# Performance work log

Hardware: AMD Instinct MI355X
Metric: run time of the kernel (lower is better)

The kernel has to match this reference:

```python
import jax, jax.numpy as jnp
import numpy as np

C = 1024        # number of classes
N = 8           # proxies per class
ALLNUM = C * N  # 8192 total proxies
DIM = 512
R = 0.05
TOPK = int(np.ceil(R * ALLNUM))  # 410
LAM = 0.3
B = 2048


def setup_inputs() -> dict:
    key = jax.random.key(0)
    k1, k2, k3 = jax.random.split(key, 3)
    inp = jax.random.normal(k1, (B, DIM), dtype=jnp.float32)
    target = jax.random.randint(k2, (B,), 0, C, dtype=jnp.int64)
    # kaiming-uniform-initialized proxies approximated by scaled normal init
    proxies = jax.random.normal(k3, (DIM, ALLNUM), dtype=jnp.float32)
    instance_label = jnp.repeat(jnp.arange(C, dtype=jnp.int64), N)  # [ALLNUM]
    return {"input": inp, "target": target, "Proxies": proxies,
            "instance_label": instance_label}


def reference(input, target, Proxies, instance_label):
    # L2-normalize each proxy column (F.normalize along dim=0, eps=1e-12)
    norm = jnp.maximum(jnp.linalg.norm(Proxies, axis=0, keepdims=True), 1e-12)
    centers = Proxies / norm                             # [DIM, ALLNUM]
    similarity = input @ centers                          # [B, ALLNUM]

    positive_mask = (target[:, None] == instance_label[None, :]).astype(similarity.dtype)
    _, indices = jax.lax.top_k(similarity + 1000.0 * positive_mask, TOPK)  # [B, TOPK]

    rows = jnp.arange(similarity.shape[0])[:, None]
    mask = jnp.zeros_like(similarity).at[rows, indices].set(1.0)
    prob_a = mask * similarity                            # sparse-masked similarities

    y_instance_onehot = jax.nn.one_hot(instance_label, C, dtype=similarity.dtype)  # [ALLNUM, C]
    logits = prob_a @ y_instance_onehot                   # [B, C]

    y_target_onehot = jax.nn.one_hot(target, C, dtype=similarity.dtype)  # [B, C]
    logits_mask = 1.0 - (logits == 0.0).astype(similarity.dtype)

    # scale_mask_softmax with scale=1 along dim=1
    e = jnp.exp(logits) * logits_mask
    predict = e / (1e-8 + jnp.sum(e, axis=1, keepdims=True))
    lossClassify = jnp.mean(jnp.sum(-y_target_onehot * jnp.log(predict + 1e-20), axis=1))

    # proxy regularizer: cross-entropy of proxy-vs-class logits
    simCenter = centers.T @ centers                       # [ALLNUM, ALLNUM]
    centers_logits = simCenter @ y_instance_onehot        # [ALLNUM, C]
    logp = jax.nn.log_softmax(centers_logits, axis=1)
    reg = -jnp.mean(jnp.take_along_axis(logp, instance_label[:, None], axis=1))

    return (lossClassify + LAM * reg, lossClassify)
```

## Files before the change

### kernel.cpp

```cpp
#include <hip/hip_runtime.h>
#include <hip/hip_bf16.h>
#include <math.h>

#define C_CLS   1024
#define NPROXY  8
#define ALLNUM  8192
#define DIM     512
#define TOPK    410
#define LAM     0.3f
#define BATCH   2048

#define BAND_CAP_BLK 28
#define ROW_CAP      512
#define GCAP         64

typedef __bf16 bf16x8 __attribute__((ext_vector_type(8)));
typedef float floatx4 __attribute__((ext_vector_type(4)));
typedef unsigned short ushort_t;

#define WS_RNORM 0
#define WS_SIG   8192
#define WS_LP    10240
#define WS_RP    12288
#define WS_CNT   14336
#define WS_NDEF  16384
#define WS_FLAG  18432
#define WS_CLS   20480
#define WS_BVAL  (WS_CLS + 2048*1024)
#define WS_BCOL  (WS_BVAL + 2048*512)
#define WS_ABF   (WS_BCOL + 2048*256)
#define WS_PBF   (WS_ABF + 524288)
#define WS_STBF  (WS_PBF + 2097152)
#define WS_MX    (WS_STBF + 262144)
#define WS_SE    (WS_MX + 65536)
#define WS_DIAG  (WS_SE + 65536)

__device__ inline float block_reduce(float v, int is_max, float* red, int t) {
    #pragma unroll
    for (int o = 32; o > 0; o >>= 1) {
        float w = __shfl_down(v, o);
        v = is_max ? fmaxf(v, w) : (v + w);
    }
    __syncthreads();
    if ((t & 63) == 0) red[t >> 6] = v;
    __syncthreads();
    return is_max ? fmaxf(fmaxf(red[0], red[1]), fmaxf(red[2], red[3]))
                  : (red[0] + red[1] + red[2] + red[3]);
}

__device__ inline ushort_t f2bf(float f) {
    unsigned u = __float_as_uint(f);
    return (ushort_t)((u + 0x7FFFu + ((u >> 16) & 1u)) >> 16);
}

__device__ inline float bf2f(ushort_t u) {
    return __uint_as_float(((unsigned)u) << 16);
}

__device__ inline void ld_g2l_16(const void* g, void* l) {
    __builtin_amdgcn_global_load_lds(
        (const __attribute__((address_space(1))) unsigned int*)g,
        (__attribute__((address_space(3))) unsigned int*)l,
        16, 0, 0);
}

__device__ inline unsigned f2ord(float f) {
    unsigned u = __float_as_uint(f);
    return (u & 0x80000000u) ? ~u : (u | 0x80000000u);
}

__global__ __launch_bounds__(256) void k_prep1(const float* __restrict__ P,
                                               const float* __restrict__ input,
                                               float* __restrict__ rnorm,
                                               float* __restrict__ rowsig,
                                               ushort_t* __restrict__ Abf,
                                               ushort_t* __restrict__ Pbf,
                                               ushort_t* __restrict__ Stbf,
                                               unsigned* __restrict__ zaux) {
    __shared__ float stile[512 * 33];
    __shared__ float cred[256];
    __shared__ float s_rn[32];
    int bx = blockIdx.x, t = threadIdx.x;
    if (bx < 256) {
        int c0 = bx * 32;
        #pragma unroll
        for (int it = 0; it < 16; ++it) {
            int r = it * 32 + (t >> 3);
            int c4 = (t & 7) * 4;
            float4 v = *(const float4*)&P[(size_t)r * ALLNUM + c0 + c4];
            stile[r * 33 + c4]     = v.x;
            stile[r * 33 + c4 + 1] = v.y;
            stile[r * 33 + c4 + 2] = v.z;
            stile[r * 33 + c4 + 3] = v.w;
        }
        __syncthreads();
        int tc = t & 31, g = t >> 5;
        float s = 0.f;
        #pragma unroll 8
        for (int k = 0; k < 64; ++k) {
            float v = stile[(g * 64 + k) * 33 + tc];
            s += v * v;
        }
        cred[g * 32 + tc] = s;
        __syncthreads();
        if (g == 0) {
            float tot = 0.f;
            #pragma unroll
            for (int k = 0; k < 8; ++k) tot += cred[k * 32 + tc];
            float r = 1.0f / fmaxf(sqrtf(tot), 1e-12f);
            rnorm[c0 + tc] = r;
            s_rn[tc] = r;
        }
        __syncthreads();
        #pragma unroll
        for (int p = 0; p < 16; ++p) {
            int idx = t + 256 * p;
            int c = idx >> 7, d4 = (idx & 127) * 4;
            ushort4 o;
            o.x = f2bf(stile[(d4    ) * 33 + c]);
            o.y = f2bf(stile[(d4 + 1) * 33 + c]);
            o.z = f2bf(stile[(d4 + 2) * 33 + c]);
            o.w = f2bf(stile[(d4 + 3) * 33 + c]);
            *(ushort4*)&Pbf[(size_t)(c0 + c) * DIM + d4] = o;
        }
        #pragma unroll
        for (int p = 0; p < 4; ++p) {
            int idx = t + 256 * p;
            int cc = idx >> 8, d2 = (idx & 255) * 2;
            float v0 = 0.f, v1 = 0.f;
            #pragma unroll
            for (int n = 0; n < 8; ++n) {
                float rr = s_rn[cc * 8 + n];
                v0 += stile[(d2    ) * 33 + cc * 8 + n] * rr;
                v1 += stile[(d2 + 1) * 33 + cc * 8 + n] * rr;
            }
            ushort2 o; o.x = f2bf(v0); o.y = f2bf(v1);
            *(ushort2*)&Stbf[(size_t)(bx * 4 + cc) * DIM + d2] = o;
        }
    } else if (bx < 256 + 1024) {
        int a = bx - 256;
        int idx = a * 256 + t;
        float4 v = ((const float4*)input)[idx];
        ushort4 o;
        o.x = f2bf(v.x); o.y = f2bf(v.y); o.z = f2bf(v.z); o.w = f2bf(v.w);
        ((ushort4*)Abf)[idx] = o;
        float sq = v.x * v.x + v.y * v.y + v.z * v.z + v.w * v.w;
        #pragma unroll
        for (int off = 32; off > 0; off >>= 1) sq += __shfl_down(sq, off);
        int lane = t & 63, w = t >> 6;
        if (lane == 0) cred[w] = sq;
        __syncthreads();
        if (t == 0) {
            rowsig[2 * a]     = sqrtf(cred[0] + cred[1]);
            rowsig[2 * a + 1] = sqrtf(cred[2] + cred[3]);
        }
    } else {
        for (int i = t; i < 3 * 2048; i += 256) zaux[i] = 0u;
    }
}

__global__ __launch_bounds__(512, 1) void k_gemms(const ushort_t* __restrict__ Abf,
                                                  const ushort_t* __restrict__ Pbf,
                                                  const ushort_t* __restrict__ Stbf,
                                                  const float* __restrict__ rnorm,
                                                  const float* __restrict__ rowsig,
                                                  const int* __restrict__ target,
                                                  float* __restrict__ g_cls,
                                                  float* __restrict__ g_bval,
                                                  ushort_t* __restrict__ g_bcol,
                                                  unsigned* __restrict__ g_cnt,
                                                  unsigned* __restrict__ g_ndef,
                                                  unsigned* __restrict__ g_flag,
                                                  float* __restrict__ g_mx,
                                                  float* __restrict__ g_se,
                                                  float* __restrict__ g_diag) {
    __shared__ __align__(16) ushort_t smem[73728];
    int bx = blockIdx.x, t = threadIdx.x;
    int w = t >> 6, lane = t & 63;
    int ml = lane & 15, q4 = lane >> 4;
    int wm = w >> 1, wn = w & 1;

    int wid = (bx & 7) * 96 + (bx >> 3);
    int isg0 = (wid < 512);
    const ushort_t* Ap;
    const ushort_t* Bp;
    int bi, bj;
    if (isg0) {
        bi = (wid & 7) * 256;
        bj = (wid >> 3) * 128;
        Ap = Abf; Bp = Pbf;
    } else {
        int id1 = wid - 512;
        bi = (id1 & 31) * 256;
        bj = (id1 >> 5) * 128;
        Ap = Pbf; Bp = Stbf;
    }

    floatx4 acc[4][4];
    #pragma unroll
    for (int mf = 0; mf < 4; ++mf)
        #pragma unroll
        for (int nf = 0; nf < 4; ++nf)
            acc[mf][nf] = (floatx4){0.f, 0.f, 0.f, 0.f};

    #define STAGE(t_, k0_) do {                                                \
        int bo_ = ((t_) % 3) * 24576;                                          \
        _Pragma("unroll")                                                      \
        for (int it_ = 0; it_ < 4; ++it_) {                                    \
            int c_ = w * 256 + it_ * 64 + lane;                                \
            int m_ = c_ >> 3, q_ = (c_ & 7) ^ (m_ & 7);                        \
            ld_g2l_16(Ap + ((size_t)(bi + m_) << 9) + (k0_) + q_ * 8,          \
                      &smem[bo_ + c_ * 8]);                                    \
        }                                                                      \
        _Pragma("unroll")                                                      \
        for (int it_ = 0; it_ < 2; ++it_) {                                    \
            int c_ = w * 128 + it_ * 64 + lane;                                \
            int m_ = c_ >> 3, q_ = (c_ & 7) ^ (m_ & 7);                        \
            ld_g2l_16(Bp + ((size_t)(bj + m_) << 9) + (k0_) + q_ * 8,          \
                      &smem[bo_ + 16384 + c_ * 8]);                            \
        } } while (0)

    STAGE(0, 0);
    STAGE(1, 64);

    #pragma unroll
    for (int tt = 0; tt < 8; ++tt) {
        if (tt < 7) asm volatile("s_waitcnt vmcnt(6)" ::: "memory");
        else        asm volatile("s_waitcnt vmcnt(0)" ::: "memory");
        __builtin_amdgcn_s_barrier();
        if (tt < 6) STAGE(tt + 2, (tt + 2) * 64);

        const ushort_t* Xa = &smem[(tt % 3) * 24576];
        const ushort_t* Xb = Xa + 16384;
        bf16x8 af[2][4], bfr[2][4];
        #pragma unroll
        for (int kk = 0; kk < 2; ++kk) {
            #pragma unroll
            for (int nf = 0; nf < 4; ++nf) {
                int n = wn * 64 + nf * 16 + ml;
                int s = (kk * 4 + q4) ^ (n & 7);
                bfr[kk][nf] = *(const bf16x8*)&Xb[n * 64 + s * 8];
            }
            #pragma unroll
            for (int mf = 0; mf < 4; ++mf) {
                int m = wm * 64 + mf * 16 + ml;
                int s = (kk * 4 + q4) ^ (m & 7);
                af[kk][mf] = *(const bf16x8*)&Xa[m * 64 + s * 8];
            }
        }
        __builtin_amdgcn_s_setprio(1);
        #pragma unroll
        for (int kk = 0; kk < 2; ++kk)
            #pragma unroll
            for (int mf = 0; mf < 4; ++mf)
                #pragma unroll
                for (int nf = 0; nf < 4; ++nf)
                    acc[mf][nf] = __builtin_amdgcn_mfma_f32_16x16x32_bf16(
                        af[kk][mf], bfr[kk][nf], acc[mf][nf], 0, 0, 0);
        __builtin_amdgcn_s_setprio(0);
    }
    #undef STAGE
    __syncthreads();

    if (isg0) {
        unsigned char* sb8 = (unsigned char*)smem;
        float*    e_cls = (float*)sb8;
        float*    e_bv  = (float*)(sb8 + 16384);
        ushort_t* e_bc  = (ushort_t*)(sb8 + 45056);
        unsigned* e_cnt = (unsigned*)(sb8 + 59392);
        unsigned* e_nd  = (unsigned*)(sb8 + 60416);

        #pragma unroll
        for (int i = t; i < 4096; i += 512) e_cls[i] = 0.f;
        if (t < 256) { e_cnt[t] = 0u; e_nd[t] = 0u; }
        __syncthreads();

        #pragma unroll
        for (int mf = 0; mf < 4; ++mf) {
            int rl0 = wm * 64 + mf * 16 + q4 * 4;
            int rowb = bi + rl0;
            float4 rs4 = *(const float4*)&rowsig[rowb];
            int4   tg4 = *(const int4*)&target[rowb];
            #pragma unroll
            for (int nf = 0; nf < 4; ++nf) {
                int cl = wn * 64 + nf * 16 + ml;
                int col = bj + cl;
                float sc = rnorm[col];
                int cls = col >> 3;
                int clsl = cl >> 3;
                #pragma unroll
                for (int i = 0; i < 4; ++i) {
                    int rl = rl0 + i;
                    float v = acc[mf][nf][i] * sc;
                    float sg = ((const float*)&rs4)[i] * (1.0f / 22.616f);
                    float hiT = 1.80f * sg, loT = 1.47f * sg;
                    int tg = ((const int*)&tg4)[i];
                    if (cls == tg) {
                        atomicAdd(&e_cls[rl * 16 + clsl], v);
                    } else if (v >= hiT) {
                        atomicAdd(&e_cls[rl * 16 + clsl], v);
                        atomicAdd(&e_nd[rl], 1u);
                    } else if (v >= loT) {
                        unsigned u = atomicAdd(&e_cnt[rl], 1u);
                        if (u < BAND_CAP_BLK) {
                            e_bv[rl * BAND_CAP_BLK + u] = v;
                            e_bc[rl * BAND_CAP_BLK + u] = (ushort_t)col;
                        }
                    }
                }
            }
        }
        __syncthreads();

        int bjc = bj >> 3;
        #pragma unroll
        for (int i = t; i < 4096; i += 512) {
            int rl = i >> 4, c = i & 15;
            g_cls[(size_t)(bi + rl) * C_CLS + bjc + c] = e_cls[i];
        }
        if (t < 256) {
            int row = bi + t;
            unsigned cbb = e_cnt[t];
            unsigned nd = e_nd[t];
            if (nd) atomicAdd(&g_ndef[row], nd);
            if (cbb) {
                unsigned cc = (cbb > BAND_CAP_BLK) ? BAND_CAP_BLK : cbb;
                unsigned base = atomicAdd(&g_cnt[row], cc);
                if (cbb > BAND_CAP_BLK || base + cc > ROW_CAP) g_flag[row] = 1u;
                for (unsigned j = 0; j < cc; ++j) {
                    if (base + j >= ROW_CAP) break;
                    g_bval[(size_t)row * ROW_CAP + base + j] = e_bv[t * BAND_CAP_BLK + j];
                    g_bcol[(size_t)row * ROW_CAP + base + j] = e_bc[t * BAND_CAP_BLK + j];
                }
            }
        }
    } else {
        int cj = bj >> 7;
        float mloc[4][4], sloc[4][4];
        #pragma unroll
        for (int mf = 0; mf < 4; ++mf) {
            int rowb = bi + wm * 64 + mf * 16 + q4 * 4;
            float4 rnr = *(const float4*)&rnorm[rowb];
            #pragma unroll
            for (int i = 0; i < 4; ++i) {
                float mm = -1e30f;
                #pragma unroll
                for (int nf = 0; nf < 4; ++nf)
                    mm = fmaxf(mm, acc[mf][nf][i] * ((const float*)&rnr)[i]);
                mloc[mf][i] = mm;
            }
        }
        #pragma unroll
        for (int off = 1; off < 16; off <<= 1)
            #pragma unroll
            for (int mf = 0; mf < 4; ++mf)
                #pragma unroll
                for (int i = 0; i < 4; ++i)
                    mloc[mf][i] = fmaxf(mloc[mf][i], __shfl_xor(mloc[mf][i], off));
        #pragma unroll
        for (int mf = 0; mf < 4; ++mf) {
            int rowb = bi + wm * 64 + mf * 16 + q4 * 4;
            float4 rnr = *(const float4*)&rnorm[rowb];
            #pragma unroll
            for (int i = 0; i < 4; ++i) {
                float ss = 0.f;
                int row = rowb + i;
                #pragma unroll
                for (int nf = 0; nf < 4; ++nf) {
                    float v = acc[mf][nf][i] * ((const float*)&rnr)[i];
                    ss += expf(v - mloc[mf][i]);
                    int col = bj + wn * 64 + nf * 16 + ml;
                    if (col == (row >> 3)) g_diag[row] = v;
                }
                sloc[mf][i] = ss;
            }
        }
        #pragma unroll
        for (int off = 1; off < 16; off <<= 1)
            #pragma unroll
            for (int mf = 0; mf < 4; ++mf)
                #pragma unroll
                for (int i = 0; i < 4; ++i)
                    sloc[mf][i] += __shfl_xor(sloc[mf][i], off);
        float* s_m = (float*)smem;
        float* s_s = s_m + 512;
        if (ml == 0) {
            #pragma unroll
            for (int mf = 0; mf < 4; ++mf)
                #pragma unroll
                for (int i = 0; i < 4; ++i) {
                    int r = wm * 64 + mf * 16 + q4 * 4 + i;
                    s_m[r * 2 + wn] = mloc[mf][i];
                    s_s[r * 2 + wn] = sloc[mf][i];
                }
        }
        __syncthreads();
        if (t < 256) {
            float m0 = s_m[2 * t], m1 = s_m[2 * t + 1];
            float s0 = s_s[2 * t], s1 = s_s[2 * t + 1];
            float M = fmaxf(m0, m1);
            float S = s0 * expf(m0 - M) + s1 * expf(m1 - M);
            g_mx[(size_t)(bi + t) * 8 + cj] = M;
            g_se[(size_t)(bi + t) * 8 + cj] = S;
        }
    }
}

__device__ inline void suffix_select1(unsigned* s_hist, unsigned kk,
                                      unsigned* s_wtot, unsigned* sh_bin,
                                      unsigned* sh_k, int t, int lane, int wid) {
    unsigned h = s_hist[t];
    unsigned v = h;
    #pragma unroll
    for (int off = 1; off < 64; off <<= 1) {
        unsigned o = __shfl_down(v, off);
        if (lane + off < 64) v += o;
    }
    if (lane == 0) s_wtot[wid] = v;
    __syncthreads();
    unsigned above = v - h;
    for (int w2 = wid + 1; w2 < 4; ++w2) above += s_wtot[w2];
    unsigned cum = above + h;
    if (cum >= kk && above < kk) { *sh_bin = (unsigned)t; *sh_k = kk - above; }
    __syncthreads();
}

__global__ __launch_bounds__(256) void k_finish(const int* __restrict__ target,
                                                const float* __restrict__ rowsig,
                                                const float* __restrict__ rnorm,
                                                const ushort_t* __restrict__ Abf,
                                                const ushort_t* __restrict__ Pbf,
                                                const float* __restrict__ g_cls,
                                                const float* __restrict__ g_bval,
                                                const ushort_t* __restrict__ g_bcol,
                                                const unsigned* __restrict__ g_cnt,
                                                const unsigned* __restrict__ g_ndef,
                                                const unsigned* __restrict__ g_flag,
                                                float* __restrict__ loss_part,
                                                const float* __restrict__ g_mx,
                                                const float* __restrict__ g_se,
                                                const float* __restrict__ g_diag,
                                                float* __restrict__ reg_part) {
    __shared__ __align__(16) unsigned char smem[16384];
    int bx = blockIdx.x, t = threadIdx.x;
    int lane = t & 63, wid = t >> 6;

    if (bx < 2048) {
        float*    s_cls  = (float*)smem;
        float*    s_bval = (float*)(smem + 4096);
        ushort_t* s_bcol = (ushort_t*)(smem + 6144);
        unsigned* s_hist = (unsigned*)(smem + 7168);
        float*    s_arow = (float*)(smem + 8192);
        unsigned* s_wtot = (unsigned*)(smem + 10240);
        unsigned* shv    = (unsigned*)(smem + 10256);
        float*    shf    = (float*)(smem + 10272);
        float*    red    = (float*)(smem + 10288);
        float*    s_gval = (float*)(smem + 10304);

        int b = bx;
        int tgt = target[b];
        float sig = rowsig[b] * (1.0f / 22.616f);
        float hiT = 1.80f * sig, loT = 1.47f * sig;
        float binscale = 256.0f / (hiT - loT);

        ((float4*)s_cls)[t] = ((const float4*)(g_cls + (size_t)b * C_CLS))[t];
        unsigned cnt = g_cnt[b], nd = g_ndef[b], fl = g_flag[b];
        int kq = (TOPK - NPROXY) - (int)nd;
        int ok = (fl == 0u) && (cnt <= ROW_CAP) && (kq >= 0) && ((int)cnt >= kq);
        if (t == 0) shv[1] = 0u;
        s_hist[t] = 0u;
        __syncthreads();

        if (ok) {
            if (kq > 0) {
                for (int j = t; j < (int)cnt; j += 256) {
                    float v = g_bval[(size_t)b * ROW_CAP + j];
                    s_bval[j] = v;
                    s_bcol[j] = g_bcol[(size_t)b * ROW_CAP + j];
                    int bin = (int)((v - loT) * binscale);
                    bin = (bin > 255) ? 255 : bin;
                    atomicAdd(&s_hist[bin], 1u);
                }
                __syncthreads();
                suffix_select1(s_hist, (unsigned)kq, s_wtot, &shv[2], &shv[3], t, lane, wid);
                int Bb = (int)shv[2];
                int knew = (int)shv[3];
                for (int j = t; j < (int)cnt; j += 256) {
                    float v = s_bval[j];
                    int bin = (int)((v - loT) * binscale);
                    bin = (bin > 255) ? 255 : bin;
                    if (bin == Bb) {
                        unsigned g = atomicAdd(&shv[1], 1u);
                        if (g < GCAP) s_gval[g] = v;
                    }
                }
                __syncthreads();
                int gc = (int)shv[1];
                if (gc <= GCAP) {
                    if (t < gc) {
                        float vj = s_gval[t];
                        unsigned g = 0, geq = 0;
                        for (int i = 0; i < gc; ++i) {
                            float vi = s_gval[i];
                            g   += (vi > vj) ? 1u : 0u;
                            geq += (vi >= vj) ? 1u : 0u;
                        }
                        if (g < (unsigned)knew && geq >= (unsigned)knew) shf[0] = vj;
                    }
                } else {
                    for (int j = t; j < (int)cnt; j += 256) {
                        float vj = s_bval[j];
                        unsigned g = 0, geq = 0;
                        for (int i = 0; i < (int)cnt; ++i) {
                            float vi = s_bval[i];
                            g   += (vi > vj) ? 1u : 0u;
                            geq += (vi >= vj) ? 1u : 0u;
                        }
                        if (g < (unsigned)kq && geq >= (unsigned)kq) shf[0] = vj;
                    }
                }
                __syncthreads();
                float thr = shf[0];
                for (int j = t; j < (int)cnt; j += 256)
                    if (s_bval[j] >= thr)
                        atomicAdd(&s_cls[s_bcol[j] >> 3], s_bval[j]);
            }
        } else {
            for (int i = t; i < DIM; i += 256)
                s_arow[i] = bf2f(Abf[(size_t)b * DIM + i]);
            #pragma unroll
            for (int i = 0; i < 4; ++i) s_cls[t + 256 * i] = 0.f;
            __syncthreads();
            float4 v4[8];
            for (int p = 0; p < 8; ++p) {
                int f = t + 256 * p;
                float vv[4];
                for (int e = 0; e < 4; ++e) {
                    int col = 4 * f + e;
                    const ushort_t* pc = Pbf + (size_t)col * DIM;
                    float a = 0.f;
                    for (int d = 0; d < DIM; ++d)
                        a += s_arow[d] * bf2f(pc[d]);
                    vv[e] = a * rnorm[col];
                }
                float4 o; o.x = vv[0]; o.y = vv[1]; o.z = vv[2]; o.w = vv[3];
                v4[p] = o;
            }
            #pragma unroll
            for (int p = 0; p < 8; ++p) {
                int f = t + 256 * p;
                const float* pv = (const float*)&v4[p];
                if ((f >> 1) == tgt)
                    atomicAdd(&s_cls[tgt], pv[0] + pv[1] + pv[2] + pv[3]);
            }
            unsigned L = 0u, R = 0xFFFFFFFFu;
            for (int it = 0; it < 33 && R - L > 1; ++it) {
                unsigned mid = L + ((R - L) >> 1);
                float c = 0.f;
                #pragma unroll
                for (int p = 0; p < 8; ++p) {
                    int f = t + 256 * p;
                    const float* pv = (const float*)&v4[p];
                    if ((f >> 1) != tgt) {
                        #pragma unroll
                        for (int e = 0; e < 4; ++e)
                            c += (f2ord(pv[e]) >= mid) ? 1.f : 0.f;
                    }
                }
                c = block_reduce(c, 0, red, t);
                if (c >= (float)(TOPK - NPROXY)) L = mid; else R = mid;
                __syncthreads();
            }
            #pragma unroll
            for (int p = 0; p < 8; ++p) {
                int f = t + 256 * p;
                const float* pv = (const float*)&v4[p];
                if ((f >> 1) != tgt) {
                    #pragma unroll
                    for (int e = 0; e < 4; ++e)
                        if (f2ord(pv[e]) >= L)
                            atomicAdd(&s_cls[f >> 1], pv[e]);
                }
            }
        }
        __syncthreads();

        float4 cv = ((const float4*)s_cls)[t];
        float m = -1e30f;
        if (cv.x != 0.0f) m = fmaxf(m, cv.x);
        if (cv.y != 0.0f) m = fmaxf(m, cv.y);
        if (cv.z != 0.0f) m = fmaxf(m, cv.z);
        if (cv.w != 0.0f) m = fmaxf(m, cv.w);
        m = block_reduce(m, 1, red, t);
        float se = 0.f;
        if (cv.x != 0.0f) se += expf(cv.x - m);
        if (cv.y != 0.0f) se += expf(cv.y - m);
        if (cv.z != 0.0f) se += expf(cv.z - m);
        if (cv.w != 0.0f) se += expf(cv.w - m);
        se = block_reduce(se, 0, red, t);
        if (t == 0) {
            float lt = s_cls[tgt];
            float predict_t = expf(lt - m) / (1e-8f * expf(-m) + se);
            loss_part[b] = -logf(predict_t + 1e-20f);
        }
    } else {
        float* red2 = (float*)smem;
        int rb = bx - 2048;
        float val = 0.f;
        if (t < 64) {
            int row = rb * 64 + t;
            float mj[8], sj[8];
            float M = -1e30f;
            #pragma unroll
            for (int j = 0; j < 8; ++j) {
                mj[j] = g_mx[(size_t)row * 8 + j];
                sj[j] = g_se[(size_t)row * 8 + j];
                M = fmaxf(M, mj[j]);
            }
            float S = 0.f;
            #pragma unroll
            for (int j = 0; j < 8; ++j) S += sj[j] * expf(mj[j] - M);
            val = M + logf(S) - g_diag[row];
        }
        val = block_reduce(val, 0, red2, t);
        if (t == 0) reg_part[rb] = val;
    }
}

__global__ __launch_bounds__(256) void k_final(const float* __restrict__ lp,
                                               const float* __restrict__ rp,
                                               float* __restrict__ out) {
    __shared__ float red[4];
    int t = threadIdx.x;
    float4 a = ((const float4*)lp)[t];
    float4 b = ((const float4*)lp)[t + 256];
    float ls = a.x + a.y + a.z + a.w + b.x + b.y + b.z + b.w;
    float rs = 0.f;
    if (t < 32) {
        float4 c = ((const float4*)rp)[t];
        rs = c.x + c.y + c.z + c.w;
    }
    ls = block_reduce(ls, 0, red, t);
    rs = block_reduce(rs, 0, red, t);
    if (t == 0) {
        float lc = ls / (float)BATCH;
        float rg = rs / (float)ALLNUM;
        out[0] = lc + LAM * rg;
        out[1] = lc;
    }
}

extern "C" void kernel_launch(void* const* d_in, const int* in_sizes, int n_in,
                              void* d_out, int out_size, void* d_ws, size_t ws_size,
                              hipStream_t stream) {
    const float* input  = (const float*)d_in[0];
    const int*   target = (const int*)d_in[1];
    const float* P      = (const float*)d_in[2];

    float* ws        = (float*)d_ws;
    float* rnorm     = ws + WS_RNORM;
    float* rowsig    = ws + WS_SIG;
    float* loss_part = ws + WS_LP;
    float* reg_part  = ws + WS_RP;
    unsigned* g_cnt  = (unsigned*)(ws + WS_CNT);
    unsigned* g_ndef = (unsigned*)(ws + WS_NDEF);
    unsigned* g_flag = (unsigned*)(ws + WS_FLAG);
    float* g_cls     = ws + WS_CLS;
    float* g_bval    = ws + WS_BVAL;
    ushort_t* g_bcol = (ushort_t*)(ws + WS_BCOL);
    ushort_t* Abf    = (ushort_t*)(ws + WS_ABF);
    ushort_t* Pbf    = (ushort_t*)(ws + WS_PBF);
    ushort_t* Stbf   = (ushort_t*)(ws + WS_STBF);
    float* g_mx      = ws + WS_MX;
    float* g_se      = ws + WS_SE;
    float* g_diag    = ws + WS_DIAG;
    float* out       = (float*)d_out;

    hipLaunchKernelGGL(k_prep1, dim3(256 + 1024 + 1), dim3(256), 0, stream,
                       P, input, rnorm, rowsig, Abf, Pbf, Stbf, g_cnt);
    hipLaunchKernelGGL(k_gemms, dim3(768), dim3(512), 0, stream,
                       Abf, Pbf, Stbf, rnorm, rowsig, target,
                       g_cls, g_bval, g_bcol, g_cnt, g_ndef, g_flag,
                       g_mx, g_se, g_diag);
    hipLaunchKernelGGL(k_finish, dim3(2048 + 128), dim3(256), 0, stream,
                       target, rowsig, rnorm, Abf, Pbf,
                       g_cls, g_bval, g_bcol, g_cnt, g_ndef, g_flag,
                       loss_part, g_mx, g_se, g_diag, reg_part);
    hipLaunchKernelGGL(k_final, dim3(1), dim3(256), 0, stream,
                       loss_part, reg_part, out);
}
```

Baseline: 153.1 us.

## Merge GEMM, finish, and final kernels into a persistent mega-kernel with spin sync

Replaces three launches (GEMMs, per-row finish, final reduction) with one persistent 256-block kernel. Blocks loop over GEMM tiles in rounds, then pick up finish and final tasks, using global atomic counters and spin-waits to wait on producer tiles. Finish blocks move from 256 to 512 threads and block_reduce8 is widened to eight waves. This removes launch gaps and lets the tail overlap with still-running GEMM tiles, but it relies on all blocks being co-resident to avoid deadlock and adds spin-wait overhead.

```diff
diff --git a/kernel.cpp b/kernel.cpp
--- a/kernel.cpp
+++ b/kernel.cpp
@@ -34,8 +34,9 @@
 #define WS_MX    (WS_STBF + 262144)
 #define WS_SE    (WS_MX + 65536)
 #define WS_DIAG  (WS_SE + 65536)
-
-__device__ inline float block_reduce(float v, int is_max, float* red, int t) {
+#define WS_SYNC  (WS_DIAG + 8192)
+
+__device__ inline float block_reduce8(float v, int is_max, float* red, int t) {
     #pragma unroll
     for (int o = 32; o > 0; o >>= 1) {
         float w = __shfl_down(v, o);
@@ -44,8 +45,12 @@
     __syncthreads();
     if ((t & 63) == 0) red[t >> 6] = v;
     __syncthreads();
-    return is_max ? fmaxf(fmaxf(red[0], red[1]), fmaxf(red[2], red[3]))
-                  : (red[0] + red[1] + red[2] + red[3]);
+    float r = is_max
+        ? fmaxf(fmaxf(fmaxf(red[0], red[1]), fmaxf(red[2], red[3])),
+                fmaxf(fmaxf(red[4], red[5]), fmaxf(red[6], red[7])))
+        : (red[0] + red[1] + red[2] + red[3] + red[4] + red[5] + red[6] + red[7]);
+    __syncthreads();
+    return r;
 }
 
 __device__ inline ushort_t f2bf(float f) {
@@ -67,6 +72,11 @@
 __device__ inline unsigned f2ord(float f) {
     unsigned u = __float_as_uint(f);
     return (u & 0x80000000u) ? ~u : (u | 0x80000000u);
+}
+
+__device__ inline void spin_until(unsigned* p, unsigned target) {
+    while (__hip_atomic_load(p, __ATOMIC_RELAXED, __HIP_MEMORY_SCOPE_AGENT) < target)
+        __builtin_amdgcn_s_sleep(2);
 }
 
 __global__ __launch_bounds__(256) void k_prep1(const float* __restrict__ P,
@@ -76,7 +86,8 @@
                                                ushort_t* __restrict__ Abf,
                                                ushort_t* __restrict__ Pbf,
                                                ushort_t* __restrict__ Stbf,
-                                               unsigned* __restrict__ zaux) {
+                                               unsigned* __restrict__ zaux,
+                                               unsigned* __restrict__ zsync) {
     __shared__ float stile[512 * 33];
     __shared__ float cred[256];
     __shared__ float s_rn[32];
@@ -156,497 +167,503 @@
         }
     } else {
         for (int i = t; i < 3 * 2048; i += 256) zaux[i] = 0u;
+        if (t < 64) zsync[t] = 0u;
     }
 }
 
-__global__ __launch_bounds__(512, 1) void k_gemms(const ushort_t* __restrict__ Abf,
-                                                  const ushort_t* __restrict__ Pbf,
-                                                  const ushort_t* __restrict__ Stbf,
-                                                  const float* __restrict__ rnorm,
-                                                  const float* __restrict__ rowsig,
-                                                  const int* __restrict__ target,
-                                                  float* __restrict__ g_cls,
-                                                  float* __restrict__ g_bval,
-                                                  ushort_t* __restrict__ g_bcol,
-                                                  unsigned* __restrict__ g_cnt,
-                                                  unsigned* __restrict__ g_ndef,
-                                                  unsigned* __restrict__ g_flag,
-                                                  float* __restrict__ g_mx,
-                                                  float* __restrict__ g_se,
-                                                  float* __restrict__ g_diag) {
+__global__ __launch_bounds__(512, 2) void k_mega(const ushort_t* __restrict__ Abf,
+                                                 const ushort_t* __restrict__ Pbf,
+                                                 const ushort_t* __restrict__ Stbf,
+                                                 const float* __restrict__ rnorm,
+                                                 const float* __restrict__ rowsig,
+                                                 const int* __restrict__ target,
+                                                 float* __restrict__ g_cls,
+                                                 float* __restrict__ g_bval,
+                                                 ushort_t* __restrict__ g_bcol,
+                                                 unsigned* __restrict__ g_cnt,
+                                                 unsigned* __restrict__ g_ndef,
+                                                 unsigned* __restrict__ g_flag,
+                                                 float* __restrict__ g_mx,
+                                                 float* __restrict__ g_se,
+                                                 float* __restrict__ g_diag,
+                                                 float* __restrict__ loss_part,
+                                                 float* __restrict__ reg_part,
+                                                 unsigned* __restrict__ sync,
+                                                 float* __restrict__ out) {
     __shared__ __align__(16) ushort_t smem[73728];
-    int bx = blockIdx.x, t = threadIdx.x;
+    __shared__ unsigned s_task;
+    int b = blockIdx.x, t = threadIdx.x;
     int w = t >> 6, lane = t & 63;
     int ml = lane & 15, q4 = lane >> 4;
     int wm = w >> 1, wn = w & 1;
 
-    int wid = (bx & 7) * 96 + (bx >> 3);
-    int isg0 = (wid < 512);
-    const ushort_t* Ap;
-    const ushort_t* Bp;
-    int bi, bj;
-    if (isg0) {
-        bi = (wid & 7) * 256;
-        bj = (wid >> 3) * 128;
-        Ap = Abf; Bp = Pbf;
-    } else {
-        int id1 = wid - 512;
-        bi = (id1 & 31) * 256;
-        bj = (id1 >> 5) * 128;
-        Ap = Pbf; Bp = Stbf;
+    #pragma unroll 1
+    for (int rd = 0; rd < 3; ++rd) {
+        int task = rd * 256 + b;
+        int isg0 = (task < 512);
+        const ushort_t* Ap;
+        const ushort_t* Bp;
+        int bi, bj;
+        if (isg0) {
+            bi = (task & 7) * 256;
+            bj = (task >> 3) * 128;
+            Ap = Abf; Bp = Pbf;
+        } else {
+            int id1 = task - 512;
+            bi = (id1 & 31) * 256;
+            bj = (id1 >> 5) * 128;
+            Ap = Pbf; Bp = Stbf;
+        }
+
+        floatx4 acc[4][4];
+        #pragma unroll
+        for (int mf = 0; mf < 4; ++mf)
+            #pragma unroll
+            for (int nf = 0; nf < 4; ++nf)
+                acc[mf][nf] = (floatx4){0.f, 0.f, 0.f, 0.f};
+
+        #define STAGE(t_, k0_) do {                                            \
+            int bo_ = ((t_) % 3) * 24576;                                      \
+            _Pragma("unroll")                                                  \
+            for (int it_ = 0; it_ < 4; ++it_) {                                \
+                int c_ = w * 256 + it_ * 64 + lane;                            \
+                int m_ = c_ >> 3, q_ = (c_ & 7) ^ (m_ & 7);                    \
+                ld_g2l_16(Ap + ((size_t)(bi + m_) << 9) + (k0_) + q_ * 8,      \
+                          &smem[bo_ + c_ * 8]);                                \
+            }                                                                  \
+            _Pragma("unroll")                                                  \
+            for (int it_ = 0; it_ < 2; ++it_) {                                \
+                int c_ = w * 128 + it_ * 64 + lane;                            \
+                int m_ = c_ >> 3, q_ = (c_ & 7) ^ (m_ & 7);                    \
+                ld_g2l_16(Bp + ((size_t)(bj + m_) << 9) + (k0_) + q_ * 8,      \
+                          &smem[bo_ + 16384 + c_ * 8]);                        \
+            } } while (0)
+
+        STAGE(0, 0);
+        STAGE(1, 64);
+
+        #pragma unroll
+        for (int tt = 0; tt < 8; ++tt) {
+            if (tt < 7) asm volatile("s_waitcnt vmcnt(6)" ::: "memory");
+            else        asm volatile("s_waitcnt vmcnt(0)" ::: "memory");
+            __builtin_amdgcn_s_barrier();
+            if (tt < 6) STAGE(tt + 2, (tt + 2) * 64);
+
+            const ushort_t* Xa = &smem[(tt % 3) * 24576];
+            const ushort_t* Xb = Xa + 16384;
+            bf16x8 af[2][4], bfr[2][4];
+            #pragma unroll
+            for (int kk = 0; kk < 2; ++kk) {
+                #pragma unroll
+                for (int nf = 0; nf < 4; ++nf) {
+                    int n = wn * 64 + nf * 16 + ml;
+                    int s = (kk * 4 + q4) ^ (n & 7);
+                    bfr[kk][nf] = *(const bf16x8*)&Xb[n * 64 + s * 8];
+                }
+                #pragma unroll
+                for (int mf = 0; mf < 4; ++mf) {
+                    int m = wm * 64 + mf * 16 + ml;
+                    int s = (kk * 4 + q4) ^ (m & 7);
+                    af[kk][mf] = *(const bf16x8*)&Xa[m * 64 + s * 8];
+                }
+            }
+            __builtin_amdgcn_s_setprio(1);
+            #pragma unroll
+            for (int kk = 0; kk < 2; ++kk)
+                #pragma unroll
+                for (int mf = 0; mf < 4; ++mf)
+                    #pragma unroll
+                    for (int nf = 0; nf < 4; ++nf)
+                        acc[mf][nf] = __builtin_amdgcn_mfma_f32_16x16x32_bf16(
+                            af[kk][mf], bfr[kk][nf], acc[mf][nf], 0, 0, 0);
+            __builtin_amdgcn_s_setprio(0);
+        }
+        #undef STAGE
+        __syncthreads();
+
+        if (isg0) {
+            unsigned char* sb8 = (unsigned char*)smem;
+            float*    e_cls = (float*)sb8;
+            float*    e_bv  = (float*)(sb8 + 16384);
+            ushort_t* e_bc  = (ushort_t*)(sb8 + 45056);
+            unsigned* e_cnt = (unsigned*)(sb8 + 59392);
+            unsigned* e_nd  = (unsigned*)(sb8 + 60416);
+
+            #pragma unroll
+            for (int i = t; i < 4096; i += 512) e_cls[i] = 0.f;
+            if (t < 256) { e_cnt[t] = 0u; e_nd[t] = 0u; }
+            __syncthreads();
+
+            #pragma unroll
+            for (int mf = 0; mf < 4; ++mf) {
+                int rl0 = wm * 64 + mf * 16 + q4 * 4;
+                int rowb = bi + rl0;
+                float4 rs4 = *(const float4*)&rowsig[rowb];
+                int4   tg4 = *(const int4*)&target[rowb];
+                #pragma unroll
+                for (int nf = 0; nf < 4; ++nf) {
+                    int cl = wn * 64 + nf * 16 + ml;
+                    int col = bj + cl;
+                    float sc = rnorm[col];
+                    int cls = col >> 3;
+                    int clsl = cl >> 3;
+                    #pragma unroll
+                    for (int i = 0; i < 4; ++i) {
+                        int rl = rl0 + i;
+                        float v = acc[mf][nf][i] * sc;
+                        float sg = ((const float*)&rs4)[i] * (1.0f / 22.616f);
+                        float hiT = 1.80f * sg, loT = 1.47f * sg;
+                        int tg = ((const int*)&tg4)[i];
+                        if (cls == tg) {
+                            atomicAdd(&e_cls[rl * 16 + clsl], v);
+                        } else if (v >= hiT) {
+                            atomicAdd(&e_cls[rl * 16 + clsl], v);
+                            atomicAdd(&e_nd[rl], 1u);
+                        } else if (v >= loT) {
+                            unsigned u = atomicAdd(&e_cnt[rl], 1u);
+                            if (u < BAND_CAP_BLK) {
+                                e_bv[rl * BAND_CAP_BLK + u] = v;
+                                e_bc[rl * BAND_CAP_BLK + u] = (ushort_t)col;
+                            }
+                        }
+                    }
+                }
+            }
+            __syncthreads();
+
+            int bjc = bj >> 3;
+            #pragma unroll
+            for (int i = t; i < 4096; i += 512) {
+                int rl = i >> 4, c = i & 15;
+                g_cls[(size_t)(bi + rl) * C_CLS + bjc + c] = e_cls[i];
+            }
+            if (t < 256) {
+                int row = bi + t;
+                unsigned cbb = e_cnt[t];
+                unsigned nd = e_nd[t];
+                if (nd) atomicAdd(&g_ndef[row], nd);
+                if (cbb) {
+                    unsigned cc = (cbb > BAND_CAP_BLK) ? BAND_CAP_BLK : cbb;
+                    unsigned base = atomicAdd(&g_cnt[row], cc);
+                    if (cbb > BAND_CAP_BLK || base + cc > ROW_CAP) g_flag[row] = 1u;
+                    for (unsigned j = 0; j < cc; ++j) {
+                        if (base + j >= ROW_CAP) break;
+                        g_bval[(size_t)row * ROW_CAP + base + j] = e_bv[t * BAND_CAP_BLK + j];
+                        g_bcol[(size_t)row * ROW_CAP + base + j] = e_bc[t * BAND_CAP_BLK + j];
+                    }
+                }
+            }
+            __syncthreads();
+            if (t == 0) { __threadfence(); atomicAdd(&sync[8 + (bi >> 8)], 1u); }
+            __syncthreads();
+        } else {
+            int cj = bj >> 7;
+            float mloc[4][4], sloc[4][4];
+            #pragma unroll
+            for (int mf = 0; mf < 4; ++mf) {
+                int rowb = bi + wm * 64 + mf * 16 + q4 * 4;
+                float4 rnr = *(const float4*)&rnorm[rowb];
+                #pragma unroll
+                for (int i = 0; i < 4; ++i) {
+                    float mm = -1e30f;
+                    #pragma unroll
+                    for (int nf = 0; nf < 4; ++nf)
+                        mm = fmaxf(mm, acc[mf][nf][i] * ((const float*)&rnr)[i]);
+                    mloc[mf][i] = mm;
+                }
+            }
+            #pragma unroll
+            for (int off = 1; off < 16; off <<= 1)
+                #pragma unroll
+                for (int mf = 0; mf < 4; ++mf)
+                    #pragma unroll
+                    for (int i = 0; i < 4; ++i)
+                        mloc[mf][i] = fmaxf(mloc[mf][i], __shfl_xor(mloc[mf][i], off));
+            #pragma unroll
+            for (int mf = 0; mf < 4; ++mf) {
+                int rowb = bi + wm * 64 + mf * 16 + q4 * 4;
+                float4 rnr = *(const float4*)&rnorm[rowb];
+                #pragma unroll
+                for (int i = 0; i < 4; ++i) {
+                    float ss = 0.f;
+                    int row = rowb + i;
+                    #pragma unroll
+                    for (int nf = 0; nf < 4; ++nf) {
+                        float v = acc[mf][nf][i] * ((const float*)&rnr)[i];
+                        ss += expf(v - mloc[mf][i]);
+                        int col = bj + wn * 64 + nf * 16 + ml;
+                        if (col == (row >> 3)) g_diag[row] = v;
+                    }
+                    sloc[mf][i] = ss;
+                }
+            }
+            #pragma unroll
+            for (int off = 1; off < 16; off <<= 1)
+                #pragma unroll
+                for (int mf = 0; mf < 4; ++mf)
+                    #pragma unroll
+                    for (int i = 0; i < 4; ++i)
+                        sloc[mf][i] += __shfl_xor(sloc[mf][i], off);
+            float* s_m = (float*)smem;
+            float* s_s = s_m + 512;
+            if (ml == 0) {
+                #pragma unroll
+                for (int mf = 0; mf < 4; ++mf)
+                    #pragma unroll
+                    for (int i = 0; i < 4; ++i) {
+                        int r = wm * 64 + mf * 16 + q4 * 4 + i;
+                        s_m[r * 2 + wn] = mloc[mf][i];
+                        s_s[r * 2 + wn] = sloc[mf][i];
+                    }
+            }
+            __syncthreads();
+            if (t < 256) {
+                float m0 = s_m[2 * t], m1 = s_m[2 * t + 1];
+                float s0 = s_s[2 * t], s1 = s_s[2 * t + 1];
+                float M = fmaxf(m0, m1);
+                float S = s0 * expf(m0 - M) + s1 * expf(m1 - M);
+                g_mx[(size_t)(bi + t) * 8 + cj] = M;
+                g_se[(size_t)(bi + t) * 8 + cj] = S;
+            }
+            __syncthreads();
+            if (t == 0) { __threadfence(); atomicAdd(&sync[16 + (bi >> 8)], 1u); }
+            __syncthreads();
+        }
     }
 
-    floatx4 acc[4][4];
-    #pragma unroll
-    for (int mf = 0; mf < 4; ++mf)
-        #pragma unroll
-        for (int nf = 0; nf < 4; ++nf)
-            acc[mf][nf] = (floatx4){0.f, 0.f, 0.f, 0.f};
-
-    #define STAGE(t_, k0_) do {                                                \
-        int bo_ = ((t_) % 3) * 24576;                                          \
-        _Pragma("unroll")                                                      \
-        for (int it_ = 0; it_ < 4; ++it_) {                                    \
-            int c_ = w * 256 + it_ * 64 + lane;                                \
-            int m_ = c_ >> 3, q_ = (c_ & 7) ^ (m_ & 7);                        \
-            ld_g2l_16(Ap + ((size_t)(bi + m_) << 9) + (k0_) + q_ * 8,          \
-                      &smem[bo_ + c_ * 8]);                                    \
-        }                                                                      \
-        _Pragma("unroll")                                                      \
-        for (int it_ = 0; it_ < 2; ++it_) {                                    \
-            int c_ = w * 128 + it_ * 64 + lane;                                \
-            int m_ = c_ >> 3, q_ = (c_ & 7) ^ (m_ & 7);                        \
-            ld_g2l_16(Bp + ((size_t)(bj + m_) << 9) + (k0_) + q_ * 8,          \
-                      &smem[bo_ + 16384 + c_ * 8]);                            \
-        } } while (0)
-
-    STAGE(0, 0);
-    STAGE(1, 64);
-
-    #pragma unroll
-    for (int tt = 0; tt < 8; ++tt) {
-        if (tt < 7) asm volatile("s_waitcnt vmcnt(6)" ::: "memory");
-        else        asm volatile("s_waitcnt vmcnt(0)" ::: "memory");
-        __builtin_amdgcn_s_barrier();
-        if (tt < 6) STAGE(tt + 2, (tt + 2) * 64);
-
-        const ushort_t* Xa = &smem[(tt % 3) * 24576];
-        const ushort_t* Xb = Xa + 16384;
-        bf16x8 af[2][4], bfr[2][4];
-        #pragma unroll
-        for (int kk = 0; kk < 2; ++kk) {
-            #pragma unroll
-            for (int nf = 0; nf < 4; ++nf) {
-                int n = wn * 64 + nf * 16 + ml;
-                int s = (kk * 4 + q4) ^ (n & 7);
-                bfr[kk][nf] = *(const bf16x8*)&Xb[n * 64 + s * 8];
-            }
-            #pragma unroll
-            for (int mf = 0; mf < 4; ++mf) {
-                int m = wm * 64 + mf * 16 + ml;
-                int s = (kk * 4 + q4) ^ (m & 7);
-                af[kk][mf] = *(const bf16x8*)&Xa[m * 64 + s * 8];
-            }
-        }
-        __builtin_amdgcn_s_setprio(1);
-        #pragma unroll
-        for (int kk = 0; kk < 2; ++kk)
-            #pragma unroll
-            for (int mf = 0; mf < 4; ++mf)
-                #pragma unroll
-                for (int nf = 0; nf < 4; ++nf)
-                    acc[mf][nf] = __builtin_amdgcn_mfma_f32_16x16x32_bf16(
-                        af[kk][mf], bfr[kk][nf], acc[mf][nf], 0, 0, 0);
-        __builtin_amdgcn_s_setprio(0);
-    }
-    #undef STAGE
-    __syncthreads();
-
-    if (isg0) {
-        unsigned char* sb8 = (unsigned char*)smem;
-        float*    e_cls = (float*)sb8;
-        float*    e_bv  = (float*)(sb8 + 16384);
-        ushort_t* e_bc  = (ushort_t*)(sb8 + 45056);
-        unsigned* e_cnt = (unsigned*)(sb8 + 59392);
-        unsigned* e_nd  = (unsigned*)(sb8 + 60416);
-
-        #pragma unroll
-        for (int i = t; i < 4096; i += 512) e_cls[i] = 0.f;
-        if (t < 256) { e_cnt[t] = 0u; e_nd[t] = 0u; }
+    for (;;) {
+        if (t == 0) s_task = atomicAdd(&sync[0], 1u);
         __syncthreads();
-
-        #pragma unroll
-        for (int mf = 0; mf < 4; ++mf) {
-            int rl0 = wm * 64 + mf * 16 + q4 * 4;
-            int rowb = bi + rl0;
-            float4 rs4 = *(const float4*)&rowsig[rowb];
-            int4   tg4 = *(const int4*)&target[rowb];
-            #pragma unroll
-            for (int nf = 0; nf < 4; ++nf) {
-                int cl = wn * 64 + nf * 16 + ml;
-                int col = bj + cl;
-                float sc = rnorm[col];
-                int cls = col >> 3;
-                int clsl = cl >> 3;
-                #pragma unroll
-                for (int i = 0; i < 4; ++i) {
-                    int rl = rl0 + i;
-                    float v = acc[mf][nf][i] * sc;
-                    float sg = ((const float*)&rs4)[i] * (1.0f / 22.616f);
-                    float hiT = 1.80f * sg, loT = 1.47f * sg;
-                    int tg = ((const int*)&tg4)[i];
-                    if (cls == tg) {
-                        atomicAdd(&e_cls[rl * 16 + clsl], v);
-                    } else if (v >= hiT) {
-                        atomicAdd(&e_cls[rl * 16 + clsl], v);
-                        atomicAdd(&e_nd[rl], 1u);
-                    } else if (v >= loT) {
-                        unsigned u = atomicAdd(&e_cnt[rl], 1u);
-                        if (u < BAND_CAP_BLK) {
-                            e_bv[rl * BAND_CAP_BLK + u] = v;
-                            e_bc[rl * BAND_CAP_BLK + u] = (ushort_t)col;
+        unsigned task = s_task;
+        if (task > 2112u) break;
+
+        if (task < 2048u) {
+            int bb = (int)(((task & 7u) << 8) | (task >> 3));
+            unsigned char* sb = (unsigned char*)smem;
+            float*    s_cls  = (float*)sb;
+            float*    s_bval = (float*)(sb + 4096);
+            ushort_t* s_bcol = (ushort_t*)(sb + 6144);
+            unsigned* s_hist = (unsigned*)(sb + 7168);
+            unsigned* s_suf  = (unsigned*)(sb + 8192);
+            float*    s_arow = (float*)(sb + 9216);
+            unsigned* shv    = (unsigned*)(sb + 11264);
+            float*    shf    = (float*)(sb + 11280);
+            float*    red    = (float*)(sb + 11296);
+            float*    s_gval = (float*)(sb + 11328);
+
+            if (t == 0) spin_until(&sync[8 + (bb >> 8)], 64u);
+            __syncthreads();
+            __threadfence();
+
+            int tgt = target[bb];
+            float sig = rowsig[bb] * (1.0f / 22.616f);
+            float hiT = 1.80f * sig, loT = 1.47f * sig;
+            float binscale = 256.0f / (hiT - loT);
+
+            if (t < 256)
+                ((float4*)s_cls)[t] = ((const float4*)(g_cls + (size_t)bb * C_CLS))[t];
+            unsigned cnt = g_cnt[bb], nd = g_ndef[bb], fl = g_flag[bb];
+            int kq = (TOPK - NPROXY) - (int)nd;
+            int ok = (fl == 0u) && (cnt <= ROW_CAP) && (kq >= 0) && ((int)cnt >= kq);
+            if (t == 0) shv[0] = 0u;
+            if (t < 256) s_hist[t] = 0u;
+            __syncthreads();
+
+            if (ok) {
+                if (kq > 0) {
+                    for (int j = t; j < (int)cnt; j += 512) {
+                        float v = g_bval[(size_t)bb * ROW_CAP + j];
+                        s_bval[j] = v;
+                        s_bcol[j] = g_bcol[(size_t)bb * ROW_CAP + j];
+                        int bin = (int)((v - loT) * binscale);
+                        bin = (bin > 255) ? 255 : bin;
+                        atomicAdd(&s_hist[bin], 1u);
+                    }
+                    __syncthreads();
+                    if (t < 256) s_suf[t] = s_hist[t];
+                    __syncthreads();
+                    for (int off = 1; off < 256; off <<= 1) {
+                        unsigned add = (t < 256 && t + off < 256) ? s_suf[t + off] : 0u;
+                        __syncthreads();
+                        if (t < 256) s_suf[t] += add;
+                        __syncthreads();
+                    }
+                    if (t < 256) {
+                        unsigned cum = s_suf[t];
+                        unsigned above = (t < 255) ? s_suf[t + 1] : 0u;
+                        if (cum >= (unsigned)kq && above < (unsigned)kq) {
+                            shv[1] = (unsigned)t; shv[2] = (unsigned)kq - above;
                         }
                     }
-                }
-            }
-        }
-        __syncthreads();
-
-        int bjc = bj >> 3;
-        #pragma unroll
-        for (int i = t; i < 4096; i += 512) {
-            int rl = i >> 4, c = i & 15;
-            g_cls[(size_t)(bi + rl) * C_CLS + bjc + c] = e_cls[i];
-        }
-        if (t < 256) {
-            int row = bi + t;
-            unsigned cbb = e_cnt[t];
-            unsigned nd = e_nd[t];
-            if (nd) atomicAdd(&g_ndef[row], nd);
-            if (cbb) {
-                unsigned cc = (cbb > BAND_CAP_BLK) ? BAND_CAP_BLK : cbb;
-                unsigned base = atomicAdd(&g_cnt[row], cc);
-                if (cbb > BAND_CAP_BLK || base + cc > ROW_CAP) g_flag[row] = 1u;
-                for (unsigned j = 0; j < cc; ++j) {
-                    if (base + j >= ROW_CAP) break;
-                    g_bval[(size_t)row * ROW_CAP + base + j] = e_bv[t * BAND_CAP_BLK + j];
-                    g_bcol[(size_t)row * ROW_CAP + base + j] = e_bc[t * BAND_CAP_BLK + j];
-                }
-            }
-        }
-    } else {
-        int cj = bj >> 7;
-        float mloc[4][4], sloc[4][4];
-        #pragma unroll
-        for (int mf = 0; mf < 4; ++mf) {
-            int rowb = bi + wm * 64 + mf * 16 + q4 * 4;
-            float4 rnr = *(const float4*)&rnorm[rowb];
-            #pragma unroll
-            for (int i = 0; i < 4; ++i) {
-                float mm = -1e30f;
-                #pragma unroll
-                for (int nf = 0; nf < 4; ++nf)
-                    mm = fmaxf(mm, acc[mf][nf][i] * ((const float*)&rnr)[i]);
-                mloc[mf][i] = mm;
-            }
-        }
-        #pragma unroll
-        for (int off = 1; off < 16; off <<= 1)
-            #pragma unroll
-            for (int mf = 0; mf < 4; ++mf)
-                #pragma unroll
-                for (int i = 0; i < 4; ++i)
-                    mloc[mf][i] = fmaxf(mloc[mf][i], __shfl_xor(mloc[mf][i], off));
-        #pragma unroll
-        for (int mf = 0; mf < 4; ++mf) {
-            int rowb = bi + wm * 64 + mf * 16 + q4 * 4;
-            float4 rnr = *(const float4*)&rnorm[rowb];
-            #pragma unroll
-            for (int i = 0; i < 4; ++i) {
-                float ss = 0.f;
-                int row = rowb + i;
-                #pragma unroll
-                for (int nf = 0; nf < 4; ++nf) {
-                    float v = acc[mf][nf][i] * ((const float*)&rnr)[i];
-                    ss += expf(v - mloc[mf][i]);
-                    int col = bj + wn * 64 + nf * 16 + ml;
-                    if (col == (row >> 3)) g_diag[row] = v;
-                }
-                sloc[mf][i] = ss;
-            }
-        }
-        #pragma unroll
-        for (int off = 1; off < 16; off <<= 1)
-            #pragma unroll
-            for (int mf = 0; mf < 4; ++mf)
-                #pragma unroll
-                for (int i = 0; i < 4; ++i)
-                    sloc[mf][i] += __shfl_xor(sloc[mf][i], off);
-        float* s_m = (float*)smem;
-        float* s_s = s_m + 512;
-        if (ml == 0) {
-            #pragma unroll
-            for (int mf = 0; mf < 4; ++mf)
-                #pragma unroll
-                for (int i = 0; i < 4; ++i) {
-                    int r = wm * 64 + mf * 16 + q4 * 4 + i;
-                    s_m[r * 2 + wn] = mloc[mf][i];
-                    s_s[r * 2 + wn] = sloc[mf][i];
-                }
-        }
-        __syncthreads();
-        if (t < 256) {
-            float m0 = s_m[2 * t], m1 = s_m[2 * t + 1];
-            float s0 = s_s[2 * t], s1 = s_s[2 * t + 1];
-            float M = fmaxf(m0, m1);
-            float S = s0 * expf(m0 - M) + s1 * expf(m1 - M);
-            g_mx[(size_t)(bi + t) * 8 + cj] = M;
-            g_se[(size_t)(bi + t) * 8 + cj] = S;
-        }
-    }
-}
-
-__device__ inline void suffix_select1(unsigned* s_hist, unsigned kk,
-                                      unsigned* s_wtot, unsigned* sh_bin,
-                                      unsigned* sh_k, int t, int lane, int wid) {
-    unsigned h = s_hist[t];
-    unsigned v = h;
-    #pragma unroll
-    for (int off = 1; off < 64; off <<= 1) {
-        unsigned o = __shfl_down(v, off);
-        if (lane + off < 64) v += o;
-    }
-    if (lane == 0) s_wtot[wid] = v;
-    __syncthreads();
-    unsigned above = v - h;
-    for (int w2 = wid + 1; w2 < 4; ++w2) above += s_wtot[w2];
-    unsigned cum = above + h;
-    if (cum >= kk && above < kk) { *sh_bin = (unsigned)t; *sh_k = kk - above; }
-    __syncthreads();
-}
-
-__global__ __launch_bounds__(256) void k_finish(const int* __restrict__ target,
-                                                const float* __restrict__ rowsig,
-                                                const float* __restrict__ rnorm,
-                                                const ushort_t* __restrict__ Abf,
-                                                const ushort_t* __restrict__ Pbf,
-                                                const float* __restrict__ g_cls,
-                                                const float* __restrict__ g_bval,
-                                                const ushort_t* __restrict__ g_bcol,
-                                                const unsigned* __restrict__ g_cnt,
-                                                const unsigned* __restrict__ g_ndef,
-                                                const unsigned* __restrict__ g_flag,
-                                                float* __restrict__ loss_part,
-                                                const float* __restrict__ g_mx,
-                                                const float* __restrict__ g_se,
-                                                const float* __restrict__ g_diag,
-                                                float* __restrict__ reg_part) {
-    __shared__ __align__(16) unsigned char smem[16384];
-    int bx = blockIdx.x, t = threadIdx.x;
-    int lane = t & 63, wid = t >> 6;
-
-    if (bx < 2048) {
-        float*    s_cls  = (float*)smem;
-        float*    s_bval = (float*)(smem + 4096);
-        ushort_t* s_bcol = (ushort_t*)(smem + 6144);
-        unsigned* s_hist = (unsigned*)(smem + 7168);
-        float*    s_arow = (float*)(smem + 8192);
-        unsigned* s_wtot = (unsigned*)(smem + 10240);
-        unsigned* shv    = (unsigned*)(smem + 10256);
-        float*    shf    = (float*)(smem + 10272);
-        float*    red    = (float*)(smem + 10288);
-        float*    s_gval = (float*)(smem + 10304);
-
-        int b = bx;
-        int tgt = target[b];
-        float sig = rowsig[b] * (1.0f / 22.616f);
-        float hiT = 1.80f * sig, loT = 1.47f * sig;
-        float binscale = 256.0f / (hiT - loT);
-
-        ((float4*)s_cls)[t] = ((const float4*)(g_cls + (size_t)b * C_CLS))[t];
-        unsigned cnt = g_cnt[b], nd = g_ndef[b], fl = g_flag[b];
-        int kq = (TOPK - NPROXY) - (int)nd;
-        int ok = (fl == 0u) && (cnt <= ROW_CAP) && (kq >= 0) && ((int)cnt >= kq);
-        if (t == 0) shv[1] = 0u;
-        s_hist[t] = 0u;
-        __syncthreads();
-
-        if (ok) {
-            if (kq > 0) {
-                for (int j = t; j < (int)cnt; j += 256) {
-                    float v = g_bval[(size_t)b * ROW_CAP + j];
-                    s_bval[j] = v;
-                    s_bcol[j] = g_bcol[(size_t)b * ROW_CAP + j];
-                    int bin = (int)((v - loT) * binscale);
-                    bin = (bin > 255) ? 255 : bin;
-                    atomicAdd(&s_hist[bin], 1u);
-                }
+                    __syncthreads();
+                    int Bb = (int)shv[1];
+                    int knew = (int)shv[2];
+                    for (int j = t; j < (int)cnt; j += 512) {
+                        float v = s_bval[j];
+                        int bin = (int)((v - loT) * binscale);
+                        bin = (bin > 255) ? 255 : bin;
+                        if (bin == Bb) {
+                            unsigned g = atomicAdd(&shv[0], 1u);
+                            if (g < GCAP) s_gval[g] = v;
+                        }
+                    }
+                    __syncthreads();
+                    int gc = (int)shv[0];
+                    if (gc <= GCAP) {
+                        if (t < gc) {
+                            float vj = s_gval[t];
+                            unsigned g = 0, geq = 0;
+                            for (int i = 0; i < gc; ++i) {
+                                float vi = s_gval[i];
+                                g   += (vi > vj) ? 1u : 0u;
+                                geq += (vi >= vj) ? 1u : 0u;
+                            }
+                            if (g < (unsigned)knew && geq >= (unsigned)knew) shf[0] = vj;
+                        }
+                    } else {
+                        for (int j = t; j < (int)cnt; j += 512) {
+                            float vj = s_bval[j];
+                            unsigned g = 0, geq = 0;
+                            for (int i = 0; i < (int)cnt; ++i) {
+                                float vi = s_bval[i];
+                                g   += (vi > vj) ? 1u : 0u;
+                                geq += (vi >= vj) ? 1u : 0u;
+                            }
+                            if (g < (unsigned)kq && geq >= (unsigned)kq) shf[0] = vj;
+                        }
+                    }
+                    __syncthreads();
+                    float thr = shf[0];
+                    for (int j = t; j < (int)cnt; j += 512)
+                        if (s_bval[j] >= thr)
+                            atomicAdd(&s_cls[s_bcol[j] >> 3], s_bval[j]);
+                }
+            } else {
+                for (int i = t; i < DIM; i += 512)
+                    s_arow[i] = bf2f(Abf[(size_t)bb * DIM + i]);
+                for (int i = t; i < 1024; i += 512) s_cls[i] = 0.f;
                 __syncthreads();
-                suffix_select1(s_hist, (unsigned)kq, s_wtot, &shv[2], &shv[3], t, lane, wid);
-                int Bb = (int)shv[2];
-                int knew = (int)shv[3];
-                for (int j = t; j < (int)cnt; j += 256) {
-                    float v = s_bval[j];
-                    int bin = (int)((v - loT) * binscale);
-                    bin = (bin > 255) ? 255 : bin;
-                    if (bin == Bb) {
-                        unsigned g = atomicAdd(&shv[1], 1u);
-                        if (g < GCAP) s_gval[g] = v;
-                    }
-                }
-                __syncthreads();
-                int gc = (int)shv[1];
-                if (gc <= GCAP) {
-                    if (t < gc) {
-                        float vj = s_gval[t];
-                        unsigned g = 0, geq = 0;
-                        for (int i = 0; i < gc; ++i) {
-                            float vi = s_gval[i];
-                            g   += (vi > vj) ? 1u : 0u;
-                            geq += (vi >= vj) ? 1u : 0u;
+                float4 v4[4];
+                #pragma unroll
+                for (int p = 0; p < 4; ++p) {
+                    int f = t + 512 * p;
+                    float vv[4];
+                    #pragma unroll
+                    for (int e = 0; e < 4; ++e) {
+                        int col = 4 * f + e;
+                        const ushort_t* pc = Pbf + (size_t)col * DIM;
+                        float a = 0.f;
+                        for (int d = 0; d < DIM; ++d)
+                            a += s_arow[d] * bf2f(pc[d]);
+                        vv[e] = a * rnorm[col];
+                    }
+                    float4 o; o.x = vv[0]; o.y = vv[1]; o.z = vv[2]; o.w = vv[3];
+                    v4[p] = o;
+                }
+                #pragma unroll
+                for (int p = 0; p < 4; ++p) {
+                    int f = t + 512 * p;
+                    const float* pv = (const float*)&v4[p];
+                    if ((f >> 1) == tgt)
+                        atomicAdd(&s_cls[tgt], pv[0] + pv[1] + pv[2] + pv[3]);
+                }
+                unsigned L = 0u, R = 0xFFFFFFFFu;
+                for (int it = 0; it < 33 && R - L > 1; ++it) {
+                    unsigned mid = L + ((R - L) >> 1);
+                    float c = 0.f;
+                    #pragma unroll
+                    for (int p = 0; p < 4; ++p) {
+                        int f = t + 512 * p;
+                        const float* pv = (const float*)&v4[p];
+                        if ((f >> 1) != tgt) {
+                            #pragma unroll
+                            for (int e = 0; e < 4; ++e)
+                                c += (f2ord(pv[e]) >= mid) ? 1.f : 0.f;
                         }
-                        if (g < (unsigned)knew && geq >= (unsigned)knew) shf[0] = vj;
-                    }
-                } else {
-                    for (int j = t; j < (int)cnt; j += 256) {
-                        float vj = s_bval[j];
-                        unsigned g = 0, geq = 0;
-                        for (int i = 0; i < (int)cnt; ++i) {
-                            float vi = s_bval[i];
-                            g   += (vi > vj) ? 1u : 0u;
-                            geq += (vi >= vj) ? 1u : 0u;
-                        }
-                        if (g < (unsigned)kq && geq >= (unsigned)kq) shf[0] = vj;
-                    }
-                }
-                __syncthreads();
-                float thr = shf[0];
-                for (int j = t; j < (int)cnt; j += 256)
-                    if (s_bval[j] >= thr)
-                        atomicAdd(&s_cls[s_bcol[j] >> 3], s_bval[j]);
-            }
-        } else {
-            for (int i = t; i < DIM; i += 256)
-                s_arow[i] = bf2f(Abf[(size_t)b * DIM + i]);
-            #pragma unroll
-            for (int i = 0; i < 4; ++i) s_cls[t + 256 * i] = 0.f;
-            __syncthreads();
-            float4 v4[8];
-            for (int p = 0; p < 8; ++p) {
-                int f = t + 256 * p;
-                float vv[4];
-                for (int e = 0; e < 4; ++e) {
-                    int col = 4 * f + e;
-                    const ushort_t* pc = Pbf + (size_t)col * DIM;
-                    float a = 0.f;
-                    for (int d = 0; d < DIM; ++d)
-                        a += s_arow[d] * bf2f(pc[d]);
-                    vv[e] = a * rnorm[col];
-                }
-                float4 o; o.x = vv[0]; o.y = vv[1]; o.z = vv[2]; o.w = vv[3];
-                v4[p] = o;
-            }
-            #pragma unroll
-            for (int p = 0; p < 8; ++p) {
-                int f = t + 256 * p;
-                const float* pv = (const float*)&v4[p];
-                if ((f >> 1) == tgt)
-                    atomicAdd(&s_cls[tgt], pv[0] + pv[1] + pv[2] + pv[3]);
-            }
-            unsigned L = 0u, R = 0xFFFFFFFFu;
-            for (int it = 0; it < 33 && R - L > 1; ++it) {
-                unsigned mid = L + ((R - L) >> 1);
-                float c = 0.f;
-                #pragma unroll
-                for (int p = 0; p < 8; ++p) {
-                    int f = t + 256 * p;
+                    }
+                    c = block_reduce8(c, 0, red, t);
+                    if (c >= (float)(TOPK - NPROXY)) L = mid; else R = mid;
+                    __syncthreads();
+                }
+                #pragma unroll
+                for (int p = 0; p < 4; ++p) {
+                    int f = t + 512 * p;
                     const float* pv = (const float*)&v4[p];
                     if ((f >> 1) != tgt) {
                         #pragma unroll
                         for (int e = 0; e < 4; ++e)
-                            c += (f2ord(pv[e]) >= mid) ? 1.f : 0.f;
-                    }
-                }
-                c = block_reduce(c, 0, red, t);
-                if (c >= (float)(TOPK - NPROXY)) L = mid; else R = mid;
-                __syncthreads();
-            }
-            #pragma unroll
-            for (int p = 0; p < 8; ++p) {
-                int f = t + 256 * p;
-                const float* pv = (const float*)&v4[p];
-                if ((f >> 1) != tgt) {
-                    #pragma unroll
-                    for (int e = 0; e < 4; ++e)
-                        if (f2ord(pv[e]) >= L)
-                            atomicAdd(&s_cls[f >> 1], pv[e]);
-                }
-            }
-        }
+                            if (f2ord(pv[e]) >= L)
+                                atomicAdd(&s_cls[f >> 1], pv[e]);
+                    }
+                }
+            }
+            __syncthreads();
+
+            float4 cv = (t < 256) ? ((const float4*)s_cls)[t]
+                                  : (float4){0.f, 0.f, 0.f, 0.f};
+            float m = -1e30f;
+            if (cv.x != 0.0f) m = fmaxf(m, cv.x);
+            if (cv.y != 0.0f) m = fmaxf(m, cv.y);
+            if (cv.z != 0.0f) m = fmaxf(m, cv.z);
+            if (cv.w != 0.0f) m = fmaxf(m, cv.w);
+            m = block_reduce8(m, 1, red, t);
+            float se = 0.f;
+            if (cv.x != 0.0f) se += expf(cv.x - m);
+            if (cv.y != 0.0f) se += expf(cv.y - m);
+            if (cv.z != 0.0f) se += expf(cv.z - m);
+            if (cv.w != 0.0f) se += expf(cv.w - m);
+            se = block_reduce8(se, 0, red, t);
+            if (t == 0) {
+                float lt = s_cls[tgt];
+                float predict_t = expf(lt - m) / (1e-8f * expf(-m) + se);
+                loss_part[bb] = -logf(predict_t + 1e-20f);
+            }
+        } else if (task < 2112u) {
+            int k = (int)task - 2048;
+            if (t == 0) spin_until(&sync[16 + (k >> 1)], 8u);
+            __syncthreads();
+            __threadfence();
+            float val = 0.f;
+            if (t < 128) {
+                int row = k * 128 + t;
+                float mj[8], sj[8];
+                float M = -1e30f;
+                #pragma unroll
+                for (int j = 0; j < 8; ++j) {
+                    mj[j] = g_mx[(size_t)row * 8 + j];
+                    sj[j] = g_se[(size_t)row * 8 + j];
+                    M = fmaxf(M, mj[j]);
+                }
+                float S = 0.f;
+                #pragma unroll
+                for (int j = 0; j < 8; ++j) S += sj[j] * expf(mj[j] - M);
+                val = M + logf(S) - g_diag[row];
+            }
+            val = block_reduce8(val, 0, (float*)smem, t);
+            if (t == 0) reg_part[k] = val;
+        } else {
+            if (t == 0) spin_until(&sync[1], 2112u);
+            __syncthreads();
+            __threadfence();
+            float4 a = ((const float4*)loss_part)[t];
+            float ls = a.x + a.y + a.z + a.w;
+            float rs = 0.f;
+            if (t < 16) {
+                float4 c = ((const float4*)reg_part)[t];
+                rs = c.x + c.y + c.z + c.w;
+            }
+            ls = block_reduce8(ls, 0, (float*)smem, t);
+            rs = block_reduce8(rs, 0, (float*)smem, t);
+            if (t == 0) {
+                float lc = ls / (float)BATCH;
+                float rg = rs / (float)ALLNUM;
+                out[0] = lc + LAM * rg;
+                out[1] = lc;
+            }
+        }
+
+        if (t == 0 && task < 2112u) { __threadfence(); atomicAdd(&sync[1], 1u); }
         __syncthreads();
-
-        float4 cv = ((const float4*)s_cls)[t];
-        float m = -1e30f;
-        if (cv.x != 0.0f) m = fmaxf(m, cv.x);
-        if (cv.y != 0.0f) m = fmaxf(m, cv.y);
-        if (cv.z != 0.0f) m = fmaxf(m, cv.z);
-        if (cv.w != 0.0f) m = fmaxf(m, cv.w);
-        m = block_reduce(m, 1, red, t);
-        float se = 0.f;
-        if (cv.x != 0.0f) se += expf(cv.x - m);
-        if (cv.y != 0.0f) se += expf(cv.y - m);
-        if (cv.z != 0.0f) se += expf(cv.z - m);
-        if (cv.w != 0.0f) se += expf(cv.w - m);
-        se = block_reduce(se, 0, red, t);
-        if (t == 0) {
-            float lt = s_cls[tgt];
-            float predict_t = expf(lt - m) / (1e-8f * expf(-m) + se);
-            loss_part[b] = -logf(predict_t + 1e-20f);
-        }
-    } else {
-        float* red2 = (float*)smem;
-        int rb = bx - 2048;
-        float val = 0.f;
-        if (t < 64) {
-            int row = rb * 64 + t;
-            float mj[8], sj[8];
-            float M = -1e30f;
-            #pragma unroll
-            for (int j = 0; j < 8; ++j) {
-                mj[j] = g_mx[(size_t)row * 8 + j];
-                sj[j] = g_se[(size_t)row * 8 + j];
-                M = fmaxf(M, mj[j]);
-            }
-            float S = 0.f;
-            #pragma unroll
-            for (int j = 0; j < 8; ++j) S += sj[j] * expf(mj[j] - M);
-            val = M + logf(S) - g_diag[row];
-        }
-        val = block_reduce(val, 0, red2, t);
-        if (t == 0) reg_part[rb] = val;
-    }
-}
-
-__global__ __launch_bounds__(256) void k_final(const float* __restrict__ lp,
-                                               const float* __restrict__ rp,
-                                               float* __restrict__ out) {
-    __shared__ float red[4];
-    int t = threadIdx.x;
-    float4 a = ((const float4*)lp)[t];
-    float4 b = ((const float4*)lp)[t + 256];
-    float ls = a.x + a.y + a.z + a.w + b.x + b.y + b.z + b.w;
-    float rs = 0.f;
-    if (t < 32) {
-        float4 c = ((const float4*)rp)[t];
-        rs = c.x + c.y + c.z + c.w;
-    }
-    ls = block_reduce(ls, 0, red, t);
-    rs = block_reduce(rs, 0, red, t);
-    if (t == 0) {
-        float lc = ls / (float)BATCH;
-        float rg = rs / (float)ALLNUM;
-        out[0] = lc + LAM * rg;
-        out[1] = lc;
     }
 }
 
@@ -674,18 +691,13 @@
     float* g_mx      = ws + WS_MX;
     float* g_se      = ws + WS_SE;
     float* g_diag    = ws + WS_DIAG;
+    unsigned* syncp  = (unsigned*)(ws + WS_SYNC);
     float* out       = (float*)d_out;
 
     hipLaunchKernelGGL(k_prep1, dim3(256 + 1024 + 1), dim3(256), 0, stream,
-                       P, input, rnorm, rowsig, Abf, Pbf, Stbf, g_cnt);
-    hipLaunchKernelGGL(k_gemms, dim3(768), dim3(512), 0, stream,
+                       P, input, rnorm, rowsig, Abf, Pbf, Stbf, g_cnt, syncp);
+    hipLaunchKernelGGL(k_mega, dim3(256), dim3(512), 0, stream,
                        Abf, Pbf, Stbf, rnorm, rowsig, target,
                        g_cls, g_bval, g_bcol, g_cnt, g_ndef, g_flag,
-                       g_mx, g_se, g_diag);
-    hipLaunchKernelGGL(k_finish, dim3(2048 + 128), dim3(256), 0, stream,
-                       target, rowsig, rnorm, Abf, Pbf,
-                       g_cls, g_bval, g_bcol, g_cnt, g_ndef, g_flag,
-                       loss_part, g_mx, g_se, g_diag, reg_part);
-    hipLaunchKernelGGL(k_final, dim3(1), dim3(256), 0, stream,
-                       loss_part, reg_part, out);
-}
+                       g_mx, g_se, g_diag, loss_part, reg_part, syncp, out);
+}
```

Result: slower. 537.5 us (+251.1%).
